# Kernel optimization log

Hardware: AMD Instinct MI355X
Metric: run time of the kernel (lower is better)

The kernel has to match this reference:

```python
import jax, jax.numpy as jnp
import numpy as np

D_MODEL = 1024
N_HEADS = 16
HEAD_DIM = D_MODEL // N_HEADS
B, L = 2, 2048


def setup_inputs() -> dict:
    key = jax.random.key(0)
    ks = jax.random.split(key, 12)
    s = 1.0 / np.sqrt(D_MODEL)
    inp = {
        'q': jax.random.normal(ks[0], (B, L, D_MODEL), dtype=jnp.float32),
        'k': jax.random.normal(ks[1], (B, L, D_MODEL), dtype=jnp.float32),
        'v': jax.random.normal(ks[2], (B, L, D_MODEL), dtype=jnp.float32),
        'Wq': jax.random.uniform(ks[3], (D_MODEL, D_MODEL), jnp.float32, -s, s),
        'bq': jax.random.uniform(ks[4], (D_MODEL,), jnp.float32, -s, s),
        'Wk': jax.random.uniform(ks[5], (D_MODEL, D_MODEL), jnp.float32, -s, s),
        'bk': jax.random.uniform(ks[6], (D_MODEL,), jnp.float32, -s, s),
        'Wv': jax.random.uniform(ks[7], (D_MODEL, D_MODEL), jnp.float32, -s, s),
        'bv': jax.random.uniform(ks[8], (D_MODEL,), jnp.float32, -s, s),
        'Wo': jax.random.uniform(ks[9], (D_MODEL, D_MODEL), jnp.float32, -s, s),
        'bo': jax.random.uniform(ks[10], (D_MODEL,), jnp.float32, -s, s),
    }
    return inp


def _heads(x):
    # (B, L, D) -> (B, H, L, Dh)
    b, l, _ = x.shape
    return x.reshape(b, l, N_HEADS, HEAD_DIM).transpose(0, 2, 1, 3)


def reference(q, k, v, Wq, bq, Wk, bk, Wv, bv, Wo, bo):
    # Linear projections (torch Linear: x @ W.T + b)
    qh = _heads(q @ Wq.T + bq)
    kh = _heads(k @ Wk.T + bk)
    vh = _heads(v @ Wv.T + bv)
    scale = 1.0 / jnp.sqrt(jnp.asarray(HEAD_DIM, dtype=qh.dtype))
    scores = jnp.einsum('bhqd,bhkd->bhqk', qh, kh) * scale  # (B,H,L,L)
    attn = jax.nn.softmax(scores, axis=-1)
    out = jnp.einsum('bhqk,bhkd->bhqd', attn, vh)
    out = out.transpose(0, 2, 1, 3).reshape(q.shape[0], q.shape[1], D_MODEL)
    return out @ Wo.T + bo
```

## Files before the change

kernel.cpp:

```cpp
#include <hip/hip_runtime.h>

typedef unsigned short u16;
typedef __bf16 bf16x8 __attribute__((ext_vector_type(8)));
typedef float f32x4 __attribute__((ext_vector_type(4)));
typedef float f32x16 __attribute__((ext_vector_type(16)));
typedef unsigned short u16x8 __attribute__((ext_vector_type(8)));
typedef unsigned int u32x2 __attribute__((ext_vector_type(2)));

#define LSEQ 2048
#define DM 1024
#define NH 16
#define HD 64
#define SCALE_Q 0.1803368801111244f

__device__ __forceinline__ u16 f2bf(float f) {
  union { float f; unsigned int u; } x;
  x.f = f;
  unsigned int u = x.u;
  u += 0x7FFFu + ((u >> 16) & 1u);
  return (u16)(u >> 16);
}

__device__ __forceinline__ float fexp2(float x) {
  return __builtin_amdgcn_exp2f(x);
}

__device__ __forceinline__ void async16(const void* g, void* l) {
  __builtin_amdgcn_global_load_lds(
      (const __attribute__((address_space(1))) void*)g,
      (__attribute__((address_space(3))) void*)l, 16, 0, 0);
}

__device__ __forceinline__ f32x4 mfma16(bf16x8 a, bf16x8 b, f32x4 c) {
  return __builtin_amdgcn_mfma_f32_16x16x32_bf16(a, b, c, 0, 0, 0);
}
__device__ __forceinline__ f32x16 mfma32(bf16x8 a, bf16x8 b, f32x16 c) {
  return __builtin_amdgcn_mfma_f32_32x32x16_bf16(a, b, c, 0, 0, 0);
}

__device__ __forceinline__ unsigned cvtpk(float lo, float hi) {
  unsigned r;
  asm("v_cvt_pk_bf16_f32 %0, %1, %2" : "=v"(r) : "v"(lo), "v"(hi));
  return r;
}
__device__ __forceinline__ void pswap(unsigned &a, unsigned &b) {
  asm("v_permlane32_swap_b32 %0, %1" : "+v"(a), "+v"(b));
}
__device__ __forceinline__ bf16x8 mk8(unsigned w0, unsigned w1, unsigned w2, unsigned w3) {
  union { unsigned u[4]; bf16x8 v; } x;
  x.u[0] = w0; x.u[1] = w1; x.u[2] = w2; x.u[3] = w3;
  return x.v;
}
__device__ __forceinline__ f32x16 zero16() {
  f32x16 z;
#pragma unroll
  for (int i = 0; i < 16; ++i) z[i] = 0.f;
  return z;
}

#define WAITBAR4 do { asm volatile("s_waitcnt vmcnt(4) lgkmcnt(0)" ::: "memory"); \
                      __builtin_amdgcn_s_barrier(); } while (0)
#define WAITBAR0 do { asm volatile("s_waitcnt vmcnt(0) lgkmcnt(0)" ::: "memory"); \
                      __builtin_amdgcn_s_barrier(); } while (0)

__global__ __launch_bounds__(256) void cvt7(
    const float* __restrict__ a0, const float* __restrict__ a1,
    const float* __restrict__ a2, const float* __restrict__ a3,
    const float* __restrict__ a4, const float* __restrict__ a5,
    const float* __restrict__ a6,
    u16* __restrict__ b0, u16* __restrict__ b1, u16* __restrict__ b2,
    u16* __restrict__ b3, u16* __restrict__ b4, u16* __restrict__ b5,
    u16* __restrict__ b6)
{
  const int t = blockIdx.y;
  const float* s; u16* d; int n;
  switch (t) {
    case 0: s = a0; d = b0; n = 1 << 22; break;
    case 1: s = a1; d = b1; n = 1 << 22; break;
    case 2: s = a2; d = b2; n = 1 << 22; break;
    case 3: s = a3; d = b3; n = 1 << 20; break;
    case 4: s = a4; d = b4; n = 1 << 20; break;
    case 5: s = a5; d = b5; n = 1 << 20; break;
    default: s = a6; d = b6; n = 1 << 20; break;
  }
  const int i = (blockIdx.x * 256 + threadIdx.x) * 8;
  if (i >= n) return;
  f32x4 f0 = *(const f32x4*)(s + i);
  f32x4 f1 = *(const f32x4*)(s + i + 4);
  u16x8 h;
#pragma unroll
  for (int j = 0; j < 4; ++j) { h[j] = f2bf(f0[j]); h[4 + j] = f2bf(f1[j]); }
  *(u16x8*)(d + i) = h;
}

__global__ __launch_bounds__(256) void gemm_qkv(
    const u16* __restrict__ Xq, const u16* __restrict__ Xk, const u16* __restrict__ Xv,
    const u16* __restrict__ Wqb, const u16* __restrict__ Wkb, const u16* __restrict__ Wvb,
    const float* __restrict__ bq, const float* __restrict__ bk, const float* __restrict__ bv,
    u16* __restrict__ Qp, u16* __restrict__ Kp, u16* __restrict__ Vt)
{
  __shared__ __align__(16) u16 As[2][128 * 32];
  __shared__ __align__(16) u16 Bs[2][128 * 32];

  const int tid = threadIdx.x;
  const int lane = tid & 63;
  const int wid = tid >> 6;
  const int lr = lane & 15, lg = lane >> 4;
  const int wr = wid >> 1, wc = wid & 1;

  const int hw = blockIdx.x;
  const int bm = (hw >> 3) & 31;
  const int by = 3 * (hw & 7) + (hw >> 8);
  const int wsel = by >> 3;
  const int bn = by & 7;

  const u16* A    = (wsel == 0) ? Xq  : (wsel == 1) ? Xk  : Xv;
  const u16* Bt   = (wsel == 0) ? Wqb : (wsel == 1) ? Wkb : Wvb;
  const float* bias = (wsel == 0) ? bq : (wsel == 1) ? bk : bv;

  const int r0 = tid >> 2;
  const int c0 = ((tid & 3) ^ ((r0 >> 1) & 3)) * 8;
  const size_t arow0 = (size_t)(bm * 128 + r0) * DM;
  const size_t arow1 = (size_t)(bm * 128 + 64 + r0) * DM;
  const size_t brow0 = (size_t)(bn * 128 + r0) * DM;
  const size_t brow1 = (size_t)(bn * 128 + 64 + r0) * DM;

  const int sA = (lg ^ ((lr >> 1) & 3)) << 3;

#define GSTAGE(t, buf) do { \
    const int kk_ = (t) * 32; \
    async16(A + arow0 + kk_ + c0, &As[buf][tid * 8]); \
    async16(A + arow1 + kk_ + c0, &As[buf][2048 + tid * 8]); \
    async16(Bt + brow0 + kk_ + c0, &Bs[buf][tid * 8]); \
    async16(Bt + brow1 + kk_ + c0, &Bs[buf][2048 + tid * 8]); \
  } while (0)

  f32x4 acc[4][4];
#pragma unroll
  for (int m = 0; m < 4; ++m)
#pragma unroll
    for (int n = 0; n < 4; ++n) {
      f32x4 z = {0.f, 0.f, 0.f, 0.f};
      acc[m][n] = z;
    }

  GSTAGE(0, 0);
  __syncthreads();

  for (int kt = 0; kt < 32; ++kt) {
    const int cur = kt & 1, nxt = cur ^ 1;
    if (kt + 1 < 32) GSTAGE(kt + 1, nxt);
    bf16x8 af[4], bfr[4];
#pragma unroll
    for (int m = 0; m < 4; ++m)
      af[m] = *(const bf16x8*)&As[cur][(wr * 64 + m * 16 + lr) * 32 + sA];
#pragma unroll
    for (int n = 0; n < 4; ++n)
      bfr[n] = *(const bf16x8*)&Bs[cur][(wc * 64 + n * 16 + lr) * 32 + sA];
#pragma unroll
    for (int m = 0; m < 4; ++m)
#pragma unroll
      for (int n = 0; n < 4; ++n)
        acc[m][n] = mfma16(af[m], bfr[n], acc[m][n]);
    __syncthreads();
  }
#undef GSTAGE

  if (wsel < 2) {
    u16* Out = (wsel == 0) ? Qp : Kp;
    const float oscale = (wsel == 0) ? SCALE_Q : 1.0f;
#pragma unroll
    for (int m = 0; m < 4; ++m) {
#pragma unroll
      for (int n = 0; n < 4; ++n) {
        const int col = bn * 128 + wc * 64 + n * 16 + lr;
        const float bv_ = bias[col];
        const int h = col >> 6, d = col & 63;
#pragma unroll
        for (int r = 0; r < 4; ++r) {
          const int row = bm * 128 + wr * 64 + m * 16 + lg * 4 + r;
          const int b = row >> 11, l = row & 2047;
          Out[((size_t)(b * NH + h) * LSEQ + l) * HD + d] =
              f2bf((acc[m][n][r] + bv_) * oscale);
        }
      }
    }
  } else {
    const int row0b = bm * 128 + wr * 64 + lg * 4;
    const int b = (bm * 128) >> 11;
#pragma unroll
    for (int m = 0; m < 4; ++m) {
      const int l0 = (row0b + m * 16) & 2047;
#pragma unroll
      for (int n = 0; n < 4; ++n) {
        const int col = bn * 128 + wc * 64 + n * 16 + lr;
        const float bv_ = bias[col];
        const int h = col >> 6, d = col & 63;
        u32x2 w;
        w[0] = cvtpk(acc[m][n][0] + bv_, acc[m][n][1] + bv_);
        w[1] = cvtpk(acc[m][n][2] + bv_, acc[m][n][3] + bv_);
        *(u32x2*)&Vt[((size_t)(b * NH + h) * HD + d) * LSEQ + l0] = w;
      }
    }
  }
}

__global__ __launch_bounds__(256) void attn_fwd(
    const u16* __restrict__ Qp, const u16* __restrict__ Kp, const u16* __restrict__ Vt,
    u16* __restrict__ ctx)
{
  __shared__ __align__(16) u16 Ks[3][64 * 64];
  __shared__ __align__(16) u16 Vts[3][64 * 64];

  const int tid = threadIdx.x;
  const int wid = tid >> 6;
  const int lane = tid & 63;
  const int lq = lane & 31;
  const int h = lane >> 5;

  const int lid = blockIdx.x + (int)gridDim.x * blockIdx.y;
  const int xcd = lid & 7, slot = lid >> 3;
  const int bh = xcd * 4 + (slot >> 4);
  const int qt = slot & 15;

  const u16* Qb = Qp + (size_t)bh * (LSEQ * HD);
  const u16* Kb = Kp + (size_t)bh * (LSEQ * HD);
  const u16* Vb = Vt + (size_t)bh * (HD * LSEQ);

  const int q0 = qt * 128 + wid * 32;

  bf16x8 qf[4];
#pragma unroll
  for (int dk = 0; dk < 4; ++dk)
    qf[dk] = *(const bf16x8*)(Qb + (size_t)(q0 + lq) * HD + dk * 16 + h * 8);

  float l_run = 0.f;
  f32x16 o0 = zero16(), o1 = zero16();

  const int srow = tid >> 3;
  const int sslot = tid & 7;
  const int sswz = (sslot ^ (srow & 7)) << 3;
  const int ksrc = srow * 64 + sswz;
  const size_t vsrc0 = (size_t)srow * LSEQ + sswz;
  const size_t vsrc1 = (size_t)(srow + 32) * LSEQ + sswz;

#define ASTAGE(t, buf) do { \
    async16(Kb + (t) * 4096 + ksrc, &Ks[buf][tid * 8]); \
    async16(Kb + (t) * 4096 + 2048 + ksrc, &Ks[buf][2048 + tid * 8]); \
    async16(Vb + (t) * 64 + vsrc0, &Vts[buf][tid * 8]); \
    async16(Vb + (t) * 64 + vsrc1, &Vts[buf][2048 + tid * 8]); \
  } while (0)

  ASTAGE(0, 0);
  ASTAGE(1, 1);
  asm volatile("s_waitcnt vmcnt(4)" ::: "memory");
  __builtin_amdgcn_s_barrier();

  int cb = 0;
  for (int kt = 0; kt < LSEQ / 64; ++kt) {
    int sb = cb + 2; if (sb >= 3) sb -= 3;
    if (kt + 2 < LSEQ / 64) ASTAGE(kt + 2, sb);

    f32x16 st0 = zero16(), st1 = zero16();
    __builtin_amdgcn_s_setprio(1);
#pragma unroll
    for (int dk = 0; dk < 4; ++dk) {
      const int g = ((2 * dk + h) ^ (lq & 7)) << 3;
      bf16x8 kf0 = *(const bf16x8*)&Ks[cb][lq * 64 + g];
      bf16x8 kf1 = *(const bf16x8*)&Ks[cb][(32 + lq) * 64 + g];
      st0 = mfma32(kf0, qf[dk], st0);
      st1 = mfma32(kf1, qf[dk], st1);
    }
    __builtin_amdgcn_s_setprio(0);

    float rs = 0.f;
#pragma unroll
    for (int i = 0; i < 16; ++i) { st0[i] = fexp2(st0[i]); rs += st0[i]; }
#pragma unroll
    for (int i = 0; i < 16; ++i) { st1[i] = fexp2(st1[i]); rs += st1[i]; }
    l_run += rs;

    unsigned w[16];
#pragma unroll
    for (int m = 0; m < 4; ++m) {
      w[m * 2 + 0] = cvtpk(st0[4 * m + 0], st0[4 * m + 1]);
      w[m * 2 + 1] = cvtpk(st0[4 * m + 2], st0[4 * m + 3]);
      w[8 + m * 2 + 0] = cvtpk(st1[4 * m + 0], st1[4 * m + 1]);
      w[8 + m * 2 + 1] = cvtpk(st1[4 * m + 2], st1[4 * m + 3]);
    }
#pragma unroll
    for (int n = 0; n < 2; ++n) {
      pswap(w[n * 8 + 0], w[n * 8 + 2]);
      pswap(w[n * 8 + 1], w[n * 8 + 3]);
      pswap(w[n * 8 + 4], w[n * 8 + 6]);
      pswap(w[n * 8 + 5], w[n * 8 + 7]);
    }
    bf16x8 pa[4];
    pa[0] = mk8(w[0], w[1], w[2], w[3]);
    pa[1] = mk8(w[4], w[5], w[6], w[7]);
    pa[2] = mk8(w[8], w[9], w[10], w[11]);
    pa[3] = mk8(w[12], w[13], w[14], w[15]);

    __builtin_amdgcn_s_setprio(1);
#pragma unroll
    for (int ks = 0; ks < 4; ++ks) {
      const int g0g = ((2 * ks + h) ^ (lq & 7)) << 3;
      bf16x8 vf0 = *(const bf16x8*)&Vts[cb][lq * 64 + g0g];
      bf16x8 vf1 = *(const bf16x8*)&Vts[cb][(32 + lq) * 64 + g0g];
      o0 = mfma32(pa[ks], vf0, o0);
      o1 = mfma32(pa[ks], vf1, o1);
    }
    __builtin_amdgcn_s_setprio(0);

    if (kt < LSEQ / 64 - 1) {
      if (kt + 2 < LSEQ / 64) { WAITBAR4; } else { WAITBAR0; }
    }
    cb = (cb + 1 == 3) ? 0 : cb + 1;
  }
#undef ASTAGE

  const int b = bh >> 4, head = bh & 15;
  const float ltot = l_run + __shfl_xor(l_run, 32);
  const float linv = 1.0f / ltot;
#pragma unroll
  for (int reg = 0; reg < 16; ++reg) {
    const int row = (reg & 3) + 8 * (reg >> 2) + 4 * h;
    const float iv = __shfl(linv, row);
    const size_t base = ((size_t)(b * LSEQ + q0 + row)) * DM + head * HD;
    ctx[base + lq] = f2bf(o0[reg] * iv);
    ctx[base + 32 + lq] = f2bf(o1[reg] * iv);
  }
}

__global__ __launch_bounds__(256) void gemm_out(
    const u16* __restrict__ Actx, const u16* __restrict__ Wob,
    const float* __restrict__ bo, float* __restrict__ out)
{
  __shared__ __align__(16) u16 As[2][128 * 32];
  __shared__ __align__(16) u16 Bs[2][128 * 32];

  const int tid = threadIdx.x;
  const int lane = tid & 63;
  const int wid = tid >> 6;
  const int lr = lane & 15, lg = lane >> 4;
  const int wr = wid >> 1, wc = wid & 1;

  const int hw = blockIdx.x;
  const int bn = hw & 7;
  const int bm = hw >> 3;

  const int r0 = tid >> 2;
  const int c0 = ((tid & 3) ^ ((r0 >> 1) & 3)) * 8;
  const size_t arow0 = (size_t)(bm * 128 + r0) * DM;
  const size_t arow1 = (size_t)(bm * 128 + 64 + r0) * DM;
  const size_t brow0 = (size_t)(bn * 128 + r0) * DM;
  const size_t brow1 = (size_t)(bn * 128 + 64 + r0) * DM;

  const int sA = (lg ^ ((lr >> 1) & 3)) << 3;

#define GSTAGE(t, buf) do { \
    const int kk_ = (t) * 32; \
    async16(Actx + arow0 + kk_ + c0, &As[buf][tid * 8]); \
    async16(Actx + arow1 + kk_ + c0, &As[buf][2048 + tid * 8]); \
    async16(Wob + brow0 + kk_ + c0, &Bs[buf][tid * 8]); \
    async16(Wob + brow1 + kk_ + c0, &Bs[buf][2048 + tid * 8]); \
  } while (0)

  f32x4 acc[4][4];
#pragma unroll
  for (int m = 0; m < 4; ++m)
#pragma unroll
    for (int n = 0; n < 4; ++n) {
      f32x4 z = {0.f, 0.f, 0.f, 0.f};
      acc[m][n] = z;
    }

  GSTAGE(0, 0);
  __syncthreads();

  for (int kt = 0; kt < 32; ++kt) {
    const int cur = kt & 1, nxt = cur ^ 1;
    if (kt + 1 < 32) GSTAGE(kt + 1, nxt);
    bf16x8 af[4], bfr[4];
#pragma unroll
    for (int m = 0; m < 4; ++m)
      af[m] = *(const bf16x8*)&As[cur][(wr * 64 + m * 16 + lr) * 32 + sA];
#pragma unroll
    for (int n = 0; n < 4; ++n)
      bfr[n] = *(const bf16x8*)&Bs[cur][(wc * 64 + n * 16 + lr) * 32 + sA];
#pragma unroll
    for (int m = 0; m < 4; ++m)
#pragma unroll
      for (int n = 0; n < 4; ++n)
        acc[m][n] = mfma16(af[m], bfr[n], acc[m][n]);
    __syncthreads();
  }
#undef GSTAGE

#pragma unroll
  for (int m = 0; m < 4; ++m) {
#pragma unroll
    for (int n = 0; n < 4; ++n) {
      const int col = bn * 128 + wc * 64 + n * 16 + lr;
      const float bv_ = bo[col];
#pragma unroll
      for (int r = 0; r < 4; ++r) {
        const int row = bm * 128 + wr * 64 + m * 16 + lg * 4 + r;
        out[(size_t)row * DM + col] = acc[m][n][r] + bv_;
      }
    }
  }
}

extern "C" void kernel_launch(void* const* d_in, const int* in_sizes, int n_in,
                              void* d_out, int out_size, void* d_ws, size_t ws_size,
                              hipStream_t stream) {
  const float* q  = (const float*)d_in[0];
  const float* k  = (const float*)d_in[1];
  const float* v  = (const float*)d_in[2];
  const float* Wq = (const float*)d_in[3];
  const float* bq = (const float*)d_in[4];
  const float* Wk = (const float*)d_in[5];
  const float* bk = (const float*)d_in[6];
  const float* Wv = (const float*)d_in[7];
  const float* bv = (const float*)d_in[8];
  const float* Wo = (const float*)d_in[9];
  const float* bo = (const float*)d_in[10];
  float* out = (float*)d_out;

  u16* ws  = (u16*)d_ws;
  u16* Xqb = ws;
  u16* Xkb = Xqb + (4u << 20);
  u16* Xvb = Xkb + (4u << 20);
  u16* Wqb = Xvb + (4u << 20);
  u16* Wkb = Wqb + (1u << 20);
  u16* Wvb = Wkb + (1u << 20);
  u16* Wob = Wvb + (1u << 20);
  u16* Qp  = Wob + (1u << 20);
  u16* Kp  = Qp + (4u << 20);
  u16* Vt  = Kp + (4u << 20);
  u16* ctx = Xqb;

  cvt7<<<dim3(2048, 7), 256, 0, stream>>>(q, k, v, Wq, Wk, Wv, Wo,
                                          Xqb, Xkb, Xvb, Wqb, Wkb, Wvb, Wob);
  gemm_qkv<<<768, 256, 0, stream>>>(Xqb, Xkb, Xvb, Wqb, Wkb, Wvb,
                                    bq, bk, bv, Qp, Kp, Vt);
  attn_fwd<<<dim3(16, 32), 256, 0, stream>>>(Qp, Kp, Vt, ctx);
  gemm_out<<<256, 256, 0, stream>>>(ctx, Wob, bo, out);
}
```

Baseline: 147.9 us.

## Shrink GEMM tiles to 64x128, drop XCD block swizzle, revert attention to double buffering

Both projection GEMMs move from 128x128 to 64x128 block tiles with a plain 2D grid, which doubles the block count and halves per-wave accumulators. The XCD-aware block index remapping in the GEMMs is removed. The attention kernel goes from a three-stage K/V pipeline with partial vmcnt waits back to a two-stage double buffer with full __syncthreads. This trades less operand reuse per block and less load/compute overlap for more parallelism and smaller LDS use.

```diff
diff --git a/kernel.cpp b/kernel.cpp
--- a/kernel.cpp
+++ b/kernel.cpp
@@ -57,11 +57,6 @@
   for (int i = 0; i < 16; ++i) z[i] = 0.f;
   return z;
 }
-
-#define WAITBAR4 do { asm volatile("s_waitcnt vmcnt(4) lgkmcnt(0)" ::: "memory"); \
-                      __builtin_amdgcn_s_barrier(); } while (0)
-#define WAITBAR0 do { asm volatile("s_waitcnt vmcnt(0) lgkmcnt(0)" ::: "memory"); \
-                      __builtin_amdgcn_s_barrier(); } while (0)
 
 __global__ __launch_bounds__(256) void cvt7(
     const float* __restrict__ a0, const float* __restrict__ a1,
@@ -99,18 +94,16 @@
     const float* __restrict__ bq, const float* __restrict__ bk, const float* __restrict__ bv,
     u16* __restrict__ Qp, u16* __restrict__ Kp, u16* __restrict__ Vt)
 {
-  __shared__ __align__(16) u16 As[2][128 * 32];
+  __shared__ __align__(16) u16 As[2][64 * 32];
   __shared__ __align__(16) u16 Bs[2][128 * 32];
 
   const int tid = threadIdx.x;
   const int lane = tid & 63;
   const int wid = tid >> 6;
   const int lr = lane & 15, lg = lane >> 4;
-  const int wr = wid >> 1, wc = wid & 1;
-
-  const int hw = blockIdx.x;
-  const int bm = (hw >> 3) & 31;
-  const int by = 3 * (hw & 7) + (hw >> 8);
+
+  const int bm = blockIdx.x;
+  const int by = blockIdx.y;
   const int wsel = by >> 3;
   const int bn = by & 7;
 
@@ -120,8 +113,7 @@
 
   const int r0 = tid >> 2;
   const int c0 = ((tid & 3) ^ ((r0 >> 1) & 3)) * 8;
-  const size_t arow0 = (size_t)(bm * 128 + r0) * DM;
-  const size_t arow1 = (size_t)(bm * 128 + 64 + r0) * DM;
+  const size_t arow = (size_t)(bm * 64 + r0) * DM;
   const size_t brow0 = (size_t)(bn * 128 + r0) * DM;
   const size_t brow1 = (size_t)(bn * 128 + 64 + r0) * DM;
 
@@ -129,17 +121,16 @@
 
 #define GSTAGE(t, buf) do { \
     const int kk_ = (t) * 32; \
-    async16(A + arow0 + kk_ + c0, &As[buf][tid * 8]); \
-    async16(A + arow1 + kk_ + c0, &As[buf][2048 + tid * 8]); \
+    async16(A + arow + kk_ + c0, &As[buf][tid * 8]); \
     async16(Bt + brow0 + kk_ + c0, &Bs[buf][tid * 8]); \
     async16(Bt + brow1 + kk_ + c0, &Bs[buf][2048 + tid * 8]); \
   } while (0)
 
-  f32x4 acc[4][4];
+  f32x4 acc[4][2];
 #pragma unroll
   for (int m = 0; m < 4; ++m)
 #pragma unroll
-    for (int n = 0; n < 4; ++n) {
+    for (int n = 0; n < 2; ++n) {
       f32x4 z = {0.f, 0.f, 0.f, 0.f};
       acc[m][n] = z;
     }
@@ -150,17 +141,17 @@
   for (int kt = 0; kt < 32; ++kt) {
     const int cur = kt & 1, nxt = cur ^ 1;
     if (kt + 1 < 32) GSTAGE(kt + 1, nxt);
-    bf16x8 af[4], bfr[4];
+    bf16x8 af[4], bfr[2];
 #pragma unroll
     for (int m = 0; m < 4; ++m)
-      af[m] = *(const bf16x8*)&As[cur][(wr * 64 + m * 16 + lr) * 32 + sA];
-#pragma unroll
-    for (int n = 0; n < 4; ++n)
-      bfr[n] = *(const bf16x8*)&Bs[cur][(wc * 64 + n * 16 + lr) * 32 + sA];
+      af[m] = *(const bf16x8*)&As[cur][(m * 16 + lr) * 32 + sA];
+#pragma unroll
+    for (int n = 0; n < 2; ++n)
+      bfr[n] = *(const bf16x8*)&Bs[cur][(wid * 32 + n * 16 + lr) * 32 + sA];
 #pragma unroll
     for (int m = 0; m < 4; ++m)
 #pragma unroll
-      for (int n = 0; n < 4; ++n)
+      for (int n = 0; n < 2; ++n)
         acc[m][n] = mfma16(af[m], bfr[n], acc[m][n]);
     __syncthreads();
   }
@@ -172,13 +163,13 @@
 #pragma unroll
     for (int m = 0; m < 4; ++m) {
 #pragma unroll
-      for (int n = 0; n < 4; ++n) {
-        const int col = bn * 128 + wc * 64 + n * 16 + lr;
+      for (int n = 0; n < 2; ++n) {
+        const int col = bn * 128 + wid * 32 + n * 16 + lr;
         const float bv_ = bias[col];
         const int h = col >> 6, d = col & 63;
 #pragma unroll
         for (int r = 0; r < 4; ++r) {
-          const int row = bm * 128 + wr * 64 + m * 16 + lg * 4 + r;
+          const int row = bm * 64 + m * 16 + lg * 4 + r;
           const int b = row >> 11, l = row & 2047;
           Out[((size_t)(b * NH + h) * LSEQ + l) * HD + d] =
               f2bf((acc[m][n][r] + bv_) * oscale);
@@ -186,14 +177,13 @@
       }
     }
   } else {
-    const int row0b = bm * 128 + wr * 64 + lg * 4;
-    const int b = (bm * 128) >> 11;
+    const int b = (bm * 64) >> 11;
 #pragma unroll
     for (int m = 0; m < 4; ++m) {
-      const int l0 = (row0b + m * 16) & 2047;
-#pragma unroll
-      for (int n = 0; n < 4; ++n) {
-        const int col = bn * 128 + wc * 64 + n * 16 + lr;
+      const int l0 = (bm * 64 + m * 16 + lg * 4) & 2047;
+#pragma unroll
+      for (int n = 0; n < 2; ++n) {
+        const int col = bn * 128 + wid * 32 + n * 16 + lr;
         const float bv_ = bias[col];
         const int h = col >> 6, d = col & 63;
         u32x2 w;
@@ -209,8 +199,8 @@
     const u16* __restrict__ Qp, const u16* __restrict__ Kp, const u16* __restrict__ Vt,
     u16* __restrict__ ctx)
 {
-  __shared__ __align__(16) u16 Ks[3][64 * 64];
-  __shared__ __align__(16) u16 Vts[3][64 * 64];
+  __shared__ __align__(16) u16 Ks[2][64 * 64];
+  __shared__ __align__(16) u16 Vts[2][64 * 64];
 
   const int tid = threadIdx.x;
   const int wid = tid >> 6;
@@ -252,22 +242,19 @@
   } while (0)
 
   ASTAGE(0, 0);
-  ASTAGE(1, 1);
-  asm volatile("s_waitcnt vmcnt(4)" ::: "memory");
-  __builtin_amdgcn_s_barrier();
-
-  int cb = 0;
+  __syncthreads();
+
   for (int kt = 0; kt < LSEQ / 64; ++kt) {
-    int sb = cb + 2; if (sb >= 3) sb -= 3;
-    if (kt + 2 < LSEQ / 64) ASTAGE(kt + 2, sb);
+    const int cur = kt & 1, nxt = cur ^ 1;
+    if (kt + 1 < LSEQ / 64) ASTAGE(kt + 1, nxt);
 
     f32x16 st0 = zero16(), st1 = zero16();
     __builtin_amdgcn_s_setprio(1);
 #pragma unroll
     for (int dk = 0; dk < 4; ++dk) {
       const int g = ((2 * dk + h) ^ (lq & 7)) << 3;
-      bf16x8 kf0 = *(const bf16x8*)&Ks[cb][lq * 64 + g];
-      bf16x8 kf1 = *(const bf16x8*)&Ks[cb][(32 + lq) * 64 + g];
+      bf16x8 kf0 = *(const bf16x8*)&Ks[cur][lq * 64 + g];
+      bf16x8 kf1 = *(const bf16x8*)&Ks[cur][(32 + lq) * 64 + g];
       st0 = mfma32(kf0, qf[dk], st0);
       st1 = mfma32(kf1, qf[dk], st1);
     }
@@ -305,17 +292,14 @@
 #pragma unroll
     for (int ks = 0; ks < 4; ++ks) {
       const int g0g = ((2 * ks + h) ^ (lq & 7)) << 3;
-      bf16x8 vf0 = *(const bf16x8*)&Vts[cb][lq * 64 + g0g];
-      bf16x8 vf1 = *(const bf16x8*)&Vts[cb][(32 + lq) * 64 + g0g];
+      bf16x8 vf0 = *(const bf16x8*)&Vts[cur][lq * 64 + g0g];
+      bf16x8 vf1 = *(const bf16x8*)&Vts[cur][(32 + lq) * 64 + g0g];
       o0 = mfma32(pa[ks], vf0, o0);
       o1 = mfma32(pa[ks], vf1, o1);
     }
     __builtin_amdgcn_s_setprio(0);
 
-    if (kt < LSEQ / 64 - 1) {
-      if (kt + 2 < LSEQ / 64) { WAITBAR4; } else { WAITBAR0; }
-    }
-    cb = (cb + 1 == 3) ? 0 : cb + 1;
+    __syncthreads();
   }
 #undef ASTAGE
 
@@ -336,23 +320,20 @@
     const u16* __restrict__ Actx, const u16* __restrict__ Wob,
     const float* __restrict__ bo, float* __restrict__ out)
 {
-  __shared__ __align__(16) u16 As[2][128 * 32];
+  __shared__ __align__(16) u16 As[2][64 * 32];
   __shared__ __align__(16) u16 Bs[2][128 * 32];
 
   const int tid = threadIdx.x;
   const int lane = tid & 63;
   const int wid = tid >> 6;
   const int lr = lane & 15, lg = lane >> 4;
-  const int wr = wid >> 1, wc = wid & 1;
-
-  const int hw = blockIdx.x;
-  const int bn = hw & 7;
-  const int bm = hw >> 3;
+
+  const int bm = blockIdx.x;
+  const int bn = blockIdx.y;
 
   const int r0 = tid >> 2;
   const int c0 = ((tid & 3) ^ ((r0 >> 1) & 3)) * 8;
-  const size_t arow0 = (size_t)(bm * 128 + r0) * DM;
-  const size_t arow1 = (size_t)(bm * 128 + 64 + r0) * DM;
+  const size_t arow = (size_t)(bm * 64 + r0) * DM;
   const size_t brow0 = (size_t)(bn * 128 + r0) * DM;
   const size_t brow1 = (size_t)(bn * 128 + 64 + r0) * DM;
 
@@ -360,17 +341,16 @@
 
 #define GSTAGE(t, buf) do { \
     const int kk_ = (t) * 32; \
-    async16(Actx + arow0 + kk_ + c0, &As[buf][tid * 8]); \
-    async16(Actx + arow1 + kk_ + c0, &As[buf][2048 + tid * 8]); \
+    async16(Actx + arow + kk_ + c0, &As[buf][tid * 8]); \
     async16(Wob + brow0 + kk_ + c0, &Bs[buf][tid * 8]); \
     async16(Wob + brow1 + kk_ + c0, &Bs[buf][2048 + tid * 8]); \
   } while (0)
 
-  f32x4 acc[4][4];
+  f32x4 acc[4][2];
 #pragma unroll
   for (int m = 0; m < 4; ++m)
 #pragma unroll
-    for (int n = 0; n < 4; ++n) {
+    for (int n = 0; n < 2; ++n) {
       f32x4 z = {0.f, 0.f, 0.f, 0.f};
       acc[m][n] = z;
     }
@@ -381,17 +361,17 @@
   for (int kt = 0; kt < 32; ++kt) {
     const int cur = kt & 1, nxt = cur ^ 1;
     if (kt + 1 < 32) GSTAGE(kt + 1, nxt);
-    bf16x8 af[4], bfr[4];
+    bf16x8 af[4], bfr[2];
 #pragma unroll
     for (int m = 0; m < 4; ++m)
-      af[m] = *(const bf16x8*)&As[cur][(wr * 64 + m * 16 + lr) * 32 + sA];
-#pragma unroll
-    for (int n = 0; n < 4; ++n)
-      bfr[n] = *(const bf16x8*)&Bs[cur][(wc * 64 + n * 16 + lr) * 32 + sA];
+      af[m] = *(const bf16x8*)&As[cur][(m * 16 + lr) * 32 + sA];
+#pragma unroll
+    for (int n = 0; n < 2; ++n)
+      bfr[n] = *(const bf16x8*)&Bs[cur][(wid * 32 + n * 16 + lr) * 32 + sA];
 #pragma unroll
     for (int m = 0; m < 4; ++m)
 #pragma unroll
-      for (int n = 0; n < 4; ++n)
+      for (int n = 0; n < 2; ++n)
         acc[m][n] = mfma16(af[m], bfr[n], acc[m][n]);
     __syncthreads();
   }
@@ -400,12 +380,12 @@
 #pragma unroll
   for (int m = 0; m < 4; ++m) {
 #pragma unroll
-    for (int n = 0; n < 4; ++n) {
-      const int col = bn * 128 + wc * 64 + n * 16 + lr;
+    for (int n = 0; n < 2; ++n) {
+      const int col = bn * 128 + wid * 32 + n * 16 + lr;
       const float bv_ = bo[col];
 #pragma unroll
       for (int r = 0; r < 4; ++r) {
-        const int row = bm * 128 + wr * 64 + m * 16 + lg * 4 + r;
+        const int row = bm * 64 + m * 16 + lg * 4 + r;
         out[(size_t)row * DM + col] = acc[m][n][r] + bv_;
       }
     }
@@ -443,8 +423,8 @@
 
   cvt7<<<dim3(2048, 7), 256, 0, stream>>>(q, k, v, Wq, Wk, Wv, Wo,
                                           Xqb, Xkb, Xvb, Wqb, Wkb, Wvb, Wob);
-  gemm_qkv<<<768, 256, 0, stream>>>(Xqb, Xkb, Xvb, Wqb, Wkb, Wvb,
-                                    bq, bk, bv, Qp, Kp, Vt);
+  gemm_qkv<<<dim3(64, 24), 256, 0, stream>>>(Xqb, Xkb, Xvb, Wqb, Wkb, Wvb,
+                                             bq, bk, bv, Qp, Kp, Vt);
   attn_fwd<<<dim3(16, 32), 256, 0, stream>>>(Qp, Kp, Vt, ctx);
-  gemm_out<<<256, 256, 0, stream>>>(ctx, Wob, bo, out);
-}
+  gemm_out<<<dim3(64, 8), 256, 0, stream>>>(ctx, Wob, bo, out);
+}
```

Measured after the change: 138.9 us. 6.1% less time.
